# Kernel optimization log

Hardware: AMD Instinct MI355X
Metric: run time of the kernel (lower is better)

## Reference

```python
import jax, jax.numpy as jnp
import numpy as np

B, DX, DY, H = 512, 128, 128, 512


def setup_inputs() -> dict:
    key = jax.random.key(0)
    ks = jax.random.split(key, 5)
    x = jax.random.normal(ks[0], (B, DX), dtype=jnp.float32)
    y = jax.random.normal(ks[1], (B, DY), dtype=jnp.float32)
    # torch nn.Linear-style weights [out_features, in_features], small init scale
    W1 = jax.random.normal(ks[2], (H, DX + DY), dtype=jnp.float32) * 0.05
    b1 = jnp.zeros((H,), dtype=jnp.float32)
    W2 = jax.random.normal(ks[3], (H, H), dtype=jnp.float32) * 0.05
    b2 = jnp.zeros((H,), dtype=jnp.float32)
    W3 = jax.random.normal(ks[4], (1, H), dtype=jnp.float32) * 0.05
    b3 = jnp.zeros((1,), dtype=jnp.float32)
    return {"x": x, "y": y, "W1": W1, "b1": b1, "W2": W2, "b2": b2, "W3": W3, "b3": b3}


def reference(x, y, W1, b1, W2, b2, W3, b3):
    # Original: pair (row i, col j) of the *returned* (transposed) matrix is
    # f(concat(x[i], y[j])). We fuse the B^2 concat + first Linear into two
    # B x H matmuls broadcast-summed (mathematically identical).
    dimX = x.shape[1]
    hx = jnp.einsum("id,hd->ih", x, W1[:, :dimX])          # [B, H]
    hy = jnp.einsum("jd,hd->jh", y, W1[:, dimX:])          # [B, H]
    h = jax.nn.relu(hx[:, None, :] + hy[None, :, :] + b1)   # [B, B, H]
    h = jax.nn.relu(jnp.einsum("ijh,kh->ijk", h, W2) + b2)  # [B, B, H]
    out = jnp.einsum("ijh,h->ij", h, W3[0]) + b3[0]         # [B, B]
    return out
```

## Files before the change

kernel.cpp:

```cpp
#include <hip/hip_runtime.h>
#include <hip/hip_bf16.h>

#define Bn  512
#define DXn 128
#define Hn  512

using bf16x8 = __attribute__((ext_vector_type(8))) short;
using f32x4  = __attribute__((ext_vector_type(4))) float;

static __device__ __forceinline__ unsigned int pkbf(float lo, float hi) {
    union { __hip_bfloat162 b; unsigned int u; } cv;
    cv.b = __float22bfloat162_rn(make_float2(lo, hi));
    return cv.u;
}

__global__ __launch_bounds__(256) void prep_h(
    const float* __restrict__ x, const float* __restrict__ y,
    const float* __restrict__ W1, const float* __restrict__ b1,
    float* __restrict__ hxb, float* __restrict__ hyv)
{
    const int which = blockIdx.z;
    const int i0 = blockIdx.y * 32;
    const int h0 = blockIdx.x * 64;
    const float* __restrict__ src = which ? y : x;
    float* __restrict__ dst = which ? hyv : hxb;
    const int off = which ? DXn : 0;

    __shared__ float xs[32][132];
    __shared__ float ws[64][132];
    const int t = threadIdx.x;
    #pragma unroll
    for (int it = 0; it < 4; ++it) {
        const int fi = it * 256 + t;
        const int r = fi >> 5, q = fi & 31;
        *(float4*)&xs[r][q * 4] = *(const float4*)&src[(i0 + r) * DXn + q * 4];
    }
    #pragma unroll
    for (int it = 0; it < 8; ++it) {
        const int fi = it * 256 + t;
        const int r = fi >> 5, q = fi & 31;
        *(float4*)&ws[r][q * 4] = *(const float4*)&W1[(h0 + r) * (2 * DXn) + off + q * 4];
    }
    __syncthreads();

    const int tx = t & 15;
    const int ty = t >> 4;
    float acc[2][4];
    #pragma unroll
    for (int v = 0; v < 2; ++v)
        #pragma unroll
        for (int u = 0; u < 4; ++u)
            acc[v][u] = which ? 0.0f : b1[h0 + tx + u * 16];

    #pragma unroll 4
    for (int c4 = 0; c4 < 32; ++c4) {
        const float4 xv0 = *(const float4*)&xs[ty * 2 + 0][c4 * 4];
        const float4 xv1 = *(const float4*)&xs[ty * 2 + 1][c4 * 4];
        #pragma unroll
        for (int u = 0; u < 4; ++u) {
            const float4 wv = *(const float4*)&ws[tx + u * 16][c4 * 4];
            acc[0][u] = fmaf(xv0.x, wv.x, fmaf(xv0.y, wv.y, fmaf(xv0.z, wv.z, fmaf(xv0.w, wv.w, acc[0][u]))));
            acc[1][u] = fmaf(xv1.x, wv.x, fmaf(xv1.y, wv.y, fmaf(xv1.z, wv.z, fmaf(xv1.w, wv.w, acc[1][u]))));
        }
    }
    #pragma unroll
    for (int v = 0; v < 2; ++v)
        #pragma unroll
        for (int u = 0; u < 4; ++u)
            dst[(size_t)(i0 + ty * 2 + v) * Hn + h0 + tx + u * 16] = acc[v][u];
}

__global__ __launch_bounds__(256) void prep_w2(
    const float* __restrict__ W2, unsigned short* __restrict__ w2s)
{
    const int T = blockIdx.x * 256 + threadIdx.x;
    const int l  = T & 63;
    const int hf = (T >> 6) & 15;
    const int kf = T >> 10;
    const int row = kf * 16 + (l & 15);
    const int col = hf * 32 + (l >> 4) * 8;
    const float* p = &W2[row * Hn + col];
    const float4 v0 = *(const float4*)p;
    const float4 v1 = *(const float4*)(p + 4);
    uint4 pk;
    pk.x = pkbf(v0.x, v0.y);
    pk.y = pkbf(v0.z, v0.w);
    pk.z = pkbf(v1.x, v1.y);
    pk.w = pkbf(v1.z, v1.w);
    *(uint4*)(w2s + (size_t)T * 8) = pk;
}

__global__ __launch_bounds__(512, 4) void critic_main(
    const float* __restrict__ hxb, const float* __restrict__ hyv,
    const unsigned short* __restrict__ w2s, const float* __restrict__ b2,
    const float* __restrict__ W3, const float* __restrict__ b3,
    float* __restrict__ out)
{
    __shared__ __align__(16) unsigned char smem[65536];
    unsigned short* a_lds = (unsigned short*)smem;
    float* red = (float*)smem;

    const int i   = blockIdx.y;
    const int j0  = blockIdx.x * 64;
    const int tid = threadIdx.x;
    const int w   = tid >> 6;
    const int l   = tid & 63;
    const int lg  = l >> 4;
    const int lm  = l & 15;

    {
        const int fr  = w & 3;
        const int fhb = (w >> 2) * 8;
        const int r   = fr * 16 + lm;
        const float* __restrict__ hyrow = &hyv[(size_t)(j0 + r) * Hn];
        const float* __restrict__ hxrow = &hxb[(size_t)i * Hn];
        #pragma unroll
        for (int q = 0; q < 8; ++q) {
            const int fh = fhb + q;
            const int h0 = fh * 32 + lg * 8;
            const float4 a0 = *(const float4*)(hyrow + h0);
            const float4 a1 = *(const float4*)(hyrow + h0 + 4);
            const float4 x0 = *(const float4*)(hxrow + h0);
            const float4 x1 = *(const float4*)(hxrow + h0 + 4);
            uint4 pk;
            pk.x = pkbf(fmaxf(a0.x + x0.x, 0.f), fmaxf(a0.y + x0.y, 0.f));
            pk.y = pkbf(fmaxf(a0.z + x0.z, 0.f), fmaxf(a0.w + x0.w, 0.f));
            pk.z = pkbf(fmaxf(a1.x + x1.x, 0.f), fmaxf(a1.y + x1.y, 0.f));
            pk.w = pkbf(fmaxf(a1.z + x1.z, 0.f), fmaxf(a1.w + x1.w, 0.f));
            *(uint4*)(a_lds + ((size_t)(fr * 16 + fh) * 64 + l) * 8) = pk;
        }
    }
    __syncthreads();

    f32x4 acc[4][4] = {};
    const unsigned short* __restrict__ wbase =
        w2s + (size_t)(w * 4) * 16 * 64 * 8;

    bf16x8 b[2][4];
    #pragma unroll
    for (int fj = 0; fj < 4; ++fj)
        b[0][fj] = *(const bf16x8*)(wbase + ((size_t)(fj * 16) * 64 + l) * 8);

    #pragma unroll
    for (int s = 0; s < 16; ++s) {
        const int cur = s & 1, nxt = cur ^ 1;
        if (s < 15) {
            #pragma unroll
            for (int fj = 0; fj < 4; ++fj)
                b[nxt][fj] = *(const bf16x8*)(wbase + ((size_t)(fj * 16 + s + 1) * 64 + l) * 8);
        }
        bf16x8 a[4];
        #pragma unroll
        for (int fi = 0; fi < 4; ++fi)
            a[fi] = *(const bf16x8*)(a_lds + ((size_t)(fi * 16 + s) * 64 + l) * 8);
        #pragma unroll
        for (int fi = 0; fi < 4; ++fi)
            #pragma unroll
            for (int fj = 0; fj < 4; ++fj)
                acc[fi][fj] = __builtin_amdgcn_mfma_f32_16x16x32_bf16(
                    a[fi], b[cur][fj], acc[fi][fj], 0, 0, 0);
    }

    float b2v[4], w3v[4];
    #pragma unroll
    for (int fj = 0; fj < 4; ++fj) {
        const int k = w * 64 + fj * 16 + lm;
        b2v[fj] = b2[k];
        w3v[fj] = W3[k];
    }
    float rp[4][4];
    #pragma unroll
    for (int fi = 0; fi < 4; ++fi) {
        #pragma unroll
        for (int q = 0; q < 4; ++q) {
            float ssum = 0.f;
            #pragma unroll
            for (int fj = 0; fj < 4; ++fj) {
                float c = acc[fi][fj][q] + b2v[fj];
                c = fmaxf(c, 0.f);
                ssum = fmaf(c, w3v[fj], ssum);
            }
            rp[fi][q] = ssum;
        }
    }
    #pragma unroll
    for (int m = 1; m < 16; m <<= 1) {
        #pragma unroll
        for (int fi = 0; fi < 4; ++fi)
            #pragma unroll
            for (int q = 0; q < 4; ++q)
                rp[fi][q] += __shfl_xor(rp[fi][q], m, 64);
    }

    __syncthreads();
    if (lm == 0) {
        #pragma unroll
        for (int fi = 0; fi < 4; ++fi)
            #pragma unroll
            for (int q = 0; q < 4; ++q)
                red[w * 64 + fi * 16 + lg * 4 + q] = rp[fi][q];
    }
    __syncthreads();
    if (tid < 64) {
        float ssum = 0.f;
        #pragma unroll
        for (int ww = 0; ww < 8; ++ww) ssum += red[ww * 64 + tid];
        out[(size_t)i * Bn + j0 + tid] = ssum + b3[0];
    }
}

extern "C" void kernel_launch(void* const* d_in, const int* in_sizes, int n_in,
                              void* d_out, int out_size, void* d_ws, size_t ws_size,
                              hipStream_t stream) {
    const float* x  = (const float*)d_in[0];
    const float* y  = (const float*)d_in[1];
    const float* W1 = (const float*)d_in[2];
    const float* b1 = (const float*)d_in[3];
    const float* W2 = (const float*)d_in[4];
    const float* b2 = (const float*)d_in[5];
    const float* W3 = (const float*)d_in[6];
    const float* b3 = (const float*)d_in[7];
    float* out = (float*)d_out;

    char* ws = (char*)d_ws;
    float* hxb = (float*)ws;
    float* hyv = (float*)(ws + (size_t)Bn * Hn * 4);
    unsigned short* w2s = (unsigned short*)(ws + (size_t)2 * Bn * Hn * 4);

    prep_h<<<dim3(Hn / 64, Bn / 32, 2), dim3(256), 0, stream>>>(x, y, W1, b1, hxb, hyv);
    prep_w2<<<dim3(128), dim3(256), 0, stream>>>(W2, w2s);
    critic_main<<<dim3(Bn / 64, Bn), dim3(512), 0, stream>>>(hxb, hyv, w2s, b2, W3, b3, out);
}
```

Measured before the change: 235.1 us.

## Double main kernel j-tile to 128 rows and merge prep kernels into one launch

The main kernel now handles 128 j-rows per block instead of 64. Each wave's W2 fragments loaded from global memory are therefore reused across twice as many MFMA tiles, which halves W2 global traffic per output. The cost is twice the LDS per block (128KB), twice the accumulator registers (8x4 f32x4), and a lower occupancy bound. Separately, the two prep kernels are fused into one launch with block-index dispatch to save a kernel launch.

```diff
diff --git a/kernel.cpp b/kernel.cpp
--- a/kernel.cpp
+++ b/kernel.cpp
@@ -14,21 +14,45 @@
     return cv.u;
 }
 
-__global__ __launch_bounds__(256) void prep_h(
+__global__ __launch_bounds__(256) void prep_fused(
     const float* __restrict__ x, const float* __restrict__ y,
     const float* __restrict__ W1, const float* __restrict__ b1,
-    float* __restrict__ hxb, float* __restrict__ hyv)
+    const float* __restrict__ W2,
+    float* __restrict__ hxb, float* __restrict__ hyv,
+    unsigned short* __restrict__ w2s)
 {
-    const int which = blockIdx.z;
-    const int i0 = blockIdx.y * 32;
-    const int h0 = blockIdx.x * 64;
+    const int bid = blockIdx.x;
+    const int t = threadIdx.x;
+
+    if (bid >= 256) {
+        const int T = (bid - 256) * 256 + t;
+        const int l  = T & 63;
+        const int hf = (T >> 6) & 15;
+        const int kf = T >> 10;
+        const int row = kf * 16 + (l & 15);
+        const int col = hf * 32 + (l >> 4) * 8;
+        const float* p = &W2[row * Hn + col];
+        const float4 v0 = *(const float4*)p;
+        const float4 v1 = *(const float4*)(p + 4);
+        uint4 pk;
+        pk.x = pkbf(v0.x, v0.y);
+        pk.y = pkbf(v0.z, v0.w);
+        pk.z = pkbf(v1.x, v1.y);
+        pk.w = pkbf(v1.z, v1.w);
+        *(uint4*)(w2s + (size_t)T * 8) = pk;
+        return;
+    }
+
+    const int which = bid >> 7;
+    const int rem = bid & 127;
+    const int i0 = (rem >> 3) * 32;
+    const int h0 = (rem & 7) * 64;
     const float* __restrict__ src = which ? y : x;
     float* __restrict__ dst = which ? hyv : hxb;
     const int off = which ? DXn : 0;
 
     __shared__ float xs[32][132];
     __shared__ float ws[64][132];
-    const int t = threadIdx.x;
     #pragma unroll
     for (int it = 0; it < 4; ++it) {
         const int fi = it * 256 + t;
@@ -70,38 +94,18 @@
             dst[(size_t)(i0 + ty * 2 + v) * Hn + h0 + tx + u * 16] = acc[v][u];
 }
 
-__global__ __launch_bounds__(256) void prep_w2(
-    const float* __restrict__ W2, unsigned short* __restrict__ w2s)
-{
-    const int T = blockIdx.x * 256 + threadIdx.x;
-    const int l  = T & 63;
-    const int hf = (T >> 6) & 15;
-    const int kf = T >> 10;
-    const int row = kf * 16 + (l & 15);
-    const int col = hf * 32 + (l >> 4) * 8;
-    const float* p = &W2[row * Hn + col];
-    const float4 v0 = *(const float4*)p;
-    const float4 v1 = *(const float4*)(p + 4);
-    uint4 pk;
-    pk.x = pkbf(v0.x, v0.y);
-    pk.y = pkbf(v0.z, v0.w);
-    pk.z = pkbf(v1.x, v1.y);
-    pk.w = pkbf(v1.z, v1.w);
-    *(uint4*)(w2s + (size_t)T * 8) = pk;
-}
-
-__global__ __launch_bounds__(512, 4) void critic_main(
+__global__ __launch_bounds__(512, 2) void critic_main(
     const float* __restrict__ hxb, const float* __restrict__ hyv,
     const unsigned short* __restrict__ w2s, const float* __restrict__ b2,
     const float* __restrict__ W3, const float* __restrict__ b3,
     float* __restrict__ out)
 {
-    __shared__ __align__(16) unsigned char smem[65536];
+    __shared__ __align__(16) unsigned char smem[131072];
     unsigned short* a_lds = (unsigned short*)smem;
     float* red = (float*)smem;
 
     const int i   = blockIdx.y;
-    const int j0  = blockIdx.x * 64;
+    const int j0  = blockIdx.x * 128;
     const int tid = threadIdx.x;
     const int w   = tid >> 6;
     const int l   = tid & 63;
@@ -109,15 +113,12 @@
     const int lm  = l & 15;
 
     {
-        const int fr  = w & 3;
-        const int fhb = (w >> 2) * 8;
-        const int r   = fr * 16 + lm;
+        const int r = w * 16 + lm;
         const float* __restrict__ hyrow = &hyv[(size_t)(j0 + r) * Hn];
         const float* __restrict__ hxrow = &hxb[(size_t)i * Hn];
         #pragma unroll
-        for (int q = 0; q < 8; ++q) {
-            const int fh = fhb + q;
-            const int h0 = fh * 32 + lg * 8;
+        for (int q = 0; q < 16; ++q) {
+            const int h0 = q * 32 + lg * 8;
             const float4 a0 = *(const float4*)(hyrow + h0);
             const float4 a1 = *(const float4*)(hyrow + h0 + 4);
             const float4 x0 = *(const float4*)(hxrow + h0);
@@ -127,12 +128,12 @@
             pk.y = pkbf(fmaxf(a0.z + x0.z, 0.f), fmaxf(a0.w + x0.w, 0.f));
             pk.z = pkbf(fmaxf(a1.x + x1.x, 0.f), fmaxf(a1.y + x1.y, 0.f));
             pk.w = pkbf(fmaxf(a1.z + x1.z, 0.f), fmaxf(a1.w + x1.w, 0.f));
-            *(uint4*)(a_lds + ((size_t)(fr * 16 + fh) * 64 + l) * 8) = pk;
-        }
-    }
-    __syncthreads();
-
-    f32x4 acc[4][4] = {};
+            *(uint4*)(a_lds + ((size_t)(w * 16 + q) * 64 + l) * 8) = pk;
+        }
+    }
+    __syncthreads();
+
+    f32x4 acc[8][4] = {};
     const unsigned short* __restrict__ wbase =
         w2s + (size_t)(w * 4) * 16 * 64 * 8;
 
@@ -149,12 +150,12 @@
             for (int fj = 0; fj < 4; ++fj)
                 b[nxt][fj] = *(const bf16x8*)(wbase + ((size_t)(fj * 16 + s + 1) * 64 + l) * 8);
         }
-        bf16x8 a[4];
-        #pragma unroll
-        for (int fi = 0; fi < 4; ++fi)
+        bf16x8 a[8];
+        #pragma unroll
+        for (int fi = 0; fi < 8; ++fi)
             a[fi] = *(const bf16x8*)(a_lds + ((size_t)(fi * 16 + s) * 64 + l) * 8);
         #pragma unroll
-        for (int fi = 0; fi < 4; ++fi)
+        for (int fi = 0; fi < 8; ++fi)
             #pragma unroll
             for (int fj = 0; fj < 4; ++fj)
                 acc[fi][fj] = __builtin_amdgcn_mfma_f32_16x16x32_bf16(
@@ -168,9 +169,9 @@
         b2v[fj] = b2[k];
         w3v[fj] = W3[k];
     }
-    float rp[4][4];
-    #pragma unroll
-    for (int fi = 0; fi < 4; ++fi) {
+    float rp[8][4];
+    #pragma unroll
+    for (int fi = 0; fi < 8; ++fi) {
         #pragma unroll
         for (int q = 0; q < 4; ++q) {
             float ssum = 0.f;
@@ -186,7 +187,7 @@
     #pragma unroll
     for (int m = 1; m < 16; m <<= 1) {
         #pragma unroll
-        for (int fi = 0; fi < 4; ++fi)
+        for (int fi = 0; fi < 8; ++fi)
             #pragma unroll
             for (int q = 0; q < 4; ++q)
                 rp[fi][q] += __shfl_xor(rp[fi][q], m, 64);
@@ -195,16 +196,16 @@
     __syncthreads();
     if (lm == 0) {
         #pragma unroll
-        for (int fi = 0; fi < 4; ++fi)
+        for (int fi = 0; fi < 8; ++fi)
             #pragma unroll
             for (int q = 0; q < 4; ++q)
-                red[w * 64 + fi * 16 + lg * 4 + q] = rp[fi][q];
-    }
-    __syncthreads();
-    if (tid < 64) {
+                red[w * 128 + fi * 16 + lg * 4 + q] = rp[fi][q];
+    }
+    __syncthreads();
+    if (tid < 128) {
         float ssum = 0.f;
         #pragma unroll
-        for (int ww = 0; ww < 8; ++ww) ssum += red[ww * 64 + tid];
+        for (int ww = 0; ww < 8; ++ww) ssum += red[ww * 128 + tid];
         out[(size_t)i * Bn + j0 + tid] = ssum + b3[0];
     }
 }
@@ -227,7 +228,6 @@
     float* hyv = (float*)(ws + (size_t)Bn * Hn * 4);
     unsigned short* w2s = (unsigned short*)(ws + (size_t)2 * Bn * Hn * 4);
 
-    prep_h<<<dim3(Hn / 64, Bn / 32, 2), dim3(256), 0, stream>>>(x, y, W1, b1, hxb, hyv);
-    prep_w2<<<dim3(128), dim3(256), 0, stream>>>(W2, w2s);
-    critic_main<<<dim3(Bn / 64, Bn), dim3(512), 0, stream>>>(hxb, hyv, w2s, b2, W3, b3, out);
-}
+    prep_fused<<<dim3(384), dim3(256), 0, stream>>>(x, y, W1, b1, W2, hxb, hyv, w2s);
+    critic_main<<<dim3(Bn / 128, Bn), dim3(512), 0, stream>>>(hxb, hyv, w2s, b2, W3, b3, out);
+}
```

Measured after the change: 245.8 us. 1.05x slower.
